# Kernel tuning notes

Measured on AMD Instinct MI355X. Metric: run time of the kernel, lower is better.

The kernel has to match this reference:

```python
import jax, jax.numpy as jnp
import numpy as np

B, T, STEPS = 4096, 56, 28
H, ANN, ENC, DEC = 126, 30, 20, 15
DIN = 1 + DEC + H  # decoder GRU input width = 142


def _gru_step(h, x, Wih, Whh, bih, bhh):
    # torch GRU cell math; Wih: [3H, in], Whh: [3H, H]
    gi = x @ Wih.T + bih
    gh = h @ Whh.T + bhh
    ir, iz, inn = jnp.split(gi, 3, axis=-1)
    hr, hz, hn = jnp.split(gh, 3, axis=-1)
    r = jax.nn.sigmoid(ir + hr)
    z = jax.nn.sigmoid(iz + hz)
    n = jnp.tanh(inn + r * hn)
    return (1.0 - z) * n + z * h


def setup_inputs() -> dict:
    key = jax.random.key(0)
    ks = jax.random.split(key, 23)
    p = lambda k, s: jax.random.normal(k, s, dtype=jnp.float32) * 0.08
    return {
        "ann_data": jax.random.normal(ks[0], (B, ANN), dtype=jnp.float32),
        "encoder_data": jax.random.normal(ks[1], (T, B, ENC), dtype=jnp.float32),
        "decoder_data": jax.random.normal(ks[2], (STEPS, B, DEC), dtype=jnp.float32),
        "s2h_W1": p(ks[3], (96, ANN)), "s2h_b1": p(ks[4], (96,)),
        "s2h_W2": p(ks[5], (H, 96)), "s2h_b2": p(ks[6], (H,)),
        "enc_Wih": p(ks[7], (3 * H, ENC)), "enc_Whh": p(ks[8], (3 * H, H)),
        "enc_bih": p(ks[9], (3 * H,)), "enc_bhh": p(ks[10], (3 * H,)),
        "dec_Wih": p(ks[11], (3 * H, DIN)), "dec_Whh": p(ks[12], (3 * H, H)),
        "dec_bih": p(ks[13], (3 * H,)), "dec_bhh": p(ks[14], (3 * H,)),
        "U_W": p(ks[15], (H, H)), "U_b": p(ks[16], (H,)),
        "Wl_W": p(ks[17], (H, H)), "Wl_b": p(ks[18], (H,)),
        "V_W": p(ks[19], (1, H)), "V_b": p(ks[20], (1,)),
        "h2o_W": p(ks[21], (1, H)), "h2o_b": p(ks[22], (1,)),
    }


def reference(ann_data, encoder_data, decoder_data,
              s2h_W1, s2h_b1, s2h_W2, s2h_b2,
              enc_Wih, enc_Whh, enc_bih, enc_bhh,
              dec_Wih, dec_Whh, dec_bih, dec_bhh,
              U_W, U_b, Wl_W, Wl_b, V_W, V_b, h2o_W, h2o_b):
    # static -> initial hidden: Linear(ANN,96) -> ReLU -> Linear(96,H)
    hidden = jnp.maximum(ann_data @ s2h_W1.T + s2h_b1, 0.0) @ s2h_W2.T + s2h_b2  # [B,H]

    def enc_f(h, x):
        h2 = _gru_step(h, x, enc_Wih, enc_Whh, enc_bih, enc_bhh)
        return h2, h2

    hidden, enc_out = jax.lax.scan(enc_f, hidden, encoder_data)  # enc_out: [T,B,H]

    Uo = enc_out @ U_W.T + U_b            # [T,B,H] precomputed (loop-invariant)
    gt0 = encoder_data[-1, :, 0:1]        # initial_ground, [B,1]

    def dec_f(carry, dec_x):
        h, prev = carry
        Wh = h @ Wl_W.T + Wl_b                              # [B,H]
        scores = jnp.tanh(Uo + Wh[None]) @ V_W.T + V_b      # [T,B,1]
        alpha = jax.nn.softmax(scores, axis=0)              # softmax over time
        attn = jnp.einsum('tb,tbh->bh', alpha[..., 0], enc_out)
        x = jnp.concatenate([prev, dec_x, attn], axis=1)    # [B,DIN]
        h2 = _gru_step(h, x, dec_Wih, dec_Whh, dec_bih, dec_bhh)
        out = h2 @ h2o_W.T + h2o_b                          # [B,1]
        return (h2, out), out

    _, outputs = jax.lax.scan(dec_f, (hidden, gt0), decoder_data)
    return outputs  # [STEPS, B, 1]
```

## Files before the change

### kernel.cpp

```cpp
#include <hip/hip_runtime.h>
#include <stdint.h>

typedef unsigned int u32;
typedef unsigned short u16;
typedef _Float16 f16;
typedef _Float16 f16x8 __attribute__((ext_vector_type(8)));
typedef _Float16 f16x4 __attribute__((ext_vector_type(4)));
typedef _Float16 f16x2 __attribute__((ext_vector_type(2)));
typedef float f32x4 __attribute__((ext_vector_type(4)));

constexpr int NB = 4096;
constexpr int NT = 56;
constexpr int NS = 28;
constexpr int NH = 126;
constexpr int NHP = 128;
constexpr float LOG2E = 1.4426950408889634f;

constexpr int LROW = 136;
constexpr int LB   = NT * LROW + 8;

constexpr int TJP = 120;
constexpr int TB  = 7712;

constexpr size_t OFF_H    = 0;
constexpr size_t OFF_ENC  = 2097152;
constexpr size_t OFF_UO   = OFF_ENC + 58720256;
constexpr size_t OFF_WENC = OFF_UO + 58720256;
constexpr size_t OFF_WDEC = OFF_WENC + 122880;
constexpr size_t OFF_WL   = OFF_WDEC + 221184;
constexpr size_t OFF_UW   = OFF_WL + 32768;

__device__ __forceinline__ float fexp2(float x){ return __builtin_amdgcn_exp2f(x); }
__device__ __forceinline__ float frcp (float x){ return __builtin_amdgcn_rcpf(x); }
__device__ __forceinline__ float sigm (float x){ return frcp(1.f + fexp2(-LOG2E * x)); }
__device__ __forceinline__ float ftanh(float x){ return 1.f - 2.f * frcp(1.f + fexp2(2.f * LOG2E * x)); }
__device__ __forceinline__ float asf(u32 u){ union { u32 i; float f; } v; v.i = u; return v.f; }
__device__ __forceinline__ u16 tobf(float f){ union { float f; u32 i; } v; v.f = f;
  return (u16)((v.i + 0x7fffu + ((v.i >> 16) & 1u)) >> 16); }

__global__ void k_prep(const float* __restrict__ eWih, const float* __restrict__ eWhh,
                       const float* __restrict__ dWih, const float* __restrict__ dWhh,
                       const float* __restrict__ UW,   const float* __restrict__ Wl,
                       char* __restrict__ ws)
{
  f16* wenc = (f16*)(ws + OFF_WENC);
  f16* wdec = (f16*)(ws + OFF_WDEC);
  f16* wl   = (f16*)(ws + OFF_WL);
  f16* uw   = (f16*)(ws + OFF_UW);
  const int nE = 384 * 160, nD = 384 * 288, nW = 128 * 128;
  const int total = nE + nD + nW + nW;
  for (int i = blockIdx.x * 256 + threadIdx.x; i < total; i += gridDim.x * 256) {
    int idx = i;
    if (idx < nE) {
      const int r = idx / 160, c = idx % 160;
      float v = 0.f;
      if (r < 378) {
        if (c < 20) v = eWih[r * 20 + c];
        else if (c >= 32 && c < 158) v = eWhh[r * 126 + (c - 32)];
      }
      wenc[idx] = (f16)v; continue;
    }
    idx -= nE;
    if (idx < nD) {
      const int r = idx / 288, c = idx % 288;
      float v = 0.f;
      if (r < 378) {
        if (c < 16) v = dWih[r * 142 + c];
        else if (c >= 32 && c < 158) v = dWih[r * 142 + 16 + (c - 32)];
        else if (c >= 160 && c < 286) v = dWhh[r * 126 + (c - 160)];
      }
      wdec[idx] = (f16)v; continue;
    }
    idx -= nD;
    if (idx < nW) {
      const int r = idx >> 7, c = idx & 127;
      wl[idx] = (f16)((r < 126 && c < 126) ? Wl[r * 126 + c] : 0.f);
      continue;
    }
    idx -= nW;
    { const int r = idx >> 7, c = idx & 127;
      uw[idx] = (f16)((r < 126 && c < 126) ? UW[r * 126 + c] : 0.f); }
  }
}

__global__ __launch_bounds__(256) void k_mlp(
    const float* __restrict__ ann, const float* __restrict__ W1, const float* __restrict__ b1,
    const float* __restrict__ W2, const float* __restrict__ b2, float* __restrict__ hstate)
{
  __shared__ float anns[32][33];
  __shared__ float t1s[32][101];
  const int tid = threadIdx.x;
  const int b0 = blockIdx.x * 32;
  for (int i = tid; i < 32 * 30; i += 256)
    anns[i / 30][i % 30] = ann[(b0 + i / 30) * 30 + (i % 30)];
  __syncthreads();
  const int b = tid & 31, rg = tid >> 5;
  for (int m = rg; m < 96; m += 8) {
    float a = b1[m];
    for (int k = 0; k < 30; ++k) a += W1[m * 30 + k] * anns[b][k];
    t1s[b][m] = fmaxf(a, 0.f);
  }
  __syncthreads();
  for (int j = rg; j < NHP; j += 8) {
    float a = 0.f;
    if (j < NH) {
      a = b2[j];
      for (int k = 0; k < 96; ++k) a += W2[j * 96 + k] * t1s[b][k];
    }
    hstate[(b0 + b) * NHP + j] = a;
  }
}

__global__ __launch_bounds__(512) void k_enc(
    const float* __restrict__ xenc, const f16* __restrict__ Wenc,
    const f16* __restrict__ Uw,
    const float* __restrict__ bih, const float* __restrict__ bhh,
    const float* __restrict__ Ub,
    float* __restrict__ hstate, f16* __restrict__ encO, u16* __restrict__ uoO)
{
  __shared__ f16 av[16][296];
  const int tid = threadIdx.x;
  const int wid = tid >> 6, l = tid & 63, quad = l >> 4, col = l & 15;
  const int b0 = blockIdx.x * 16;
  const int jb = wid * 16, j = jb + col;
  const bool valid = j < NH;
  const int jc = valid ? j : NH - 1;

  const float br  = bih[jc]        + bhh[jc];
  const float bz  = bih[NH + jc]   + bhh[NH + jc];
  const float bnx = bih[2*NH + jc];
  const float bnh = bhh[2*NH + jc];
  const float ub  = Ub[jc];

  f16x8 rB[5], zB[5], nxB, nhB[4], uB[4];
  {
    const int ko = quad * 8, rr = jb + col;
#pragma unroll
    for (int kt = 0; kt < 5; ++kt) {
      rB[kt] = *(const f16x8*)&Wenc[rr * 160 + kt * 32 + ko];
      zB[kt] = *(const f16x8*)&Wenc[(NH + rr) * 160 + kt * 32 + ko];
    }
    nxB = *(const f16x8*)&Wenc[(2*NH + rr) * 160 + ko];
#pragma unroll
    for (int kt = 0; kt < 4; ++kt) {
      nhB[kt] = *(const f16x8*)&Wenc[(2*NH + rr) * 160 + 32 + kt * 32 + ko];
      uB[kt]  = *(const f16x8*)&Uw[rr * 128 + kt * 32 + ko];
    }
  }

  {
    const int bb = tid >> 5, c4 = (tid & 31) * 4;
    const float4 hv = *(const float4*)&hstate[(b0 + bb) * NHP + c4];
    av[bb][32 + c4]     = (f16)hv.x; av[bb][32 + c4 + 1] = (f16)hv.y;
    av[bb][32 + c4 + 2] = (f16)hv.z; av[bb][32 + c4 + 3] = (f16)hv.w;
  }
  if (tid < 192) { const int bb = tid / 12, p = tid % 12; av[bb][20 + p] = (f16)0.f; }
  __syncthreads();

  const int m = col, ko = quad * 8;
  for (int t = 0; t < NT; ++t) {
    const int hp = 32 + (t & 1) * 128, hq = 32 + ((t + 1) & 1) * 128;
    if (tid < 320) {
      const int bb = tid / 20, e = tid % 20;
      av[bb][e] = (f16)xenc[((size_t)t * NB + b0 + bb) * 20 + e];
    }
    __syncthreads();
    f16x8 A[5];
    A[0] = *(const f16x8*)&av[m][ko];
#pragma unroll
    for (int kt = 1; kt < 5; ++kt) A[kt] = *(const f16x8*)&av[m][hp + (kt - 1) * 32 + ko];

    f32x4 Cr = {br, br, br, br}, Cz = {bz, bz, bz, bz};
    f32x4 Cnx = {bnx, bnx, bnx, bnx}, Cnh = {bnh, bnh, bnh, bnh};
#pragma unroll
    for (int kt = 0; kt < 5; ++kt) {
      Cr = __builtin_amdgcn_mfma_f32_16x16x32_f16(A[kt], rB[kt], Cr, 0, 0, 0);
      Cz = __builtin_amdgcn_mfma_f32_16x16x32_f16(A[kt], zB[kt], Cz, 0, 0, 0);
    }
    Cnx = __builtin_amdgcn_mfma_f32_16x16x32_f16(A[0], nxB, Cnx, 0, 0, 0);
#pragma unroll
    for (int kt = 0; kt < 4; ++kt)
      Cnh = __builtin_amdgcn_mfma_f32_16x16x32_f16(A[kt + 1], nhB[kt], Cnh, 0, 0, 0);

    float hv4[4];
#pragma unroll
    for (int c = 0; c < 4; ++c) {
      const int bb = quad * 4 + c;
      const float hold = (float)av[bb][hp + j];
      const float r = sigm(Cr[c]), z = sigm(Cz[c]);
      const float n = ftanh(Cnx[c] + r * Cnh[c]);
      hv4[c] = (1.f - z) * n + z * hold;
    }
#pragma unroll
    for (int c = 0; c < 4; ++c) {
      const int bb = quad * 4 + c;
      const f16 hs = valid ? (f16)hv4[c] : (f16)0.f;
      av[bb][hq + j] = hs;
      encO[((size_t)(b0 + bb) * NT + t) * 128 + j] = hs;
    }
    if (t == NT - 1 && valid) {
#pragma unroll
      for (int c = 0; c < 4; ++c)
        hstate[(b0 + quad * 4 + c) * NHP + j] = hv4[c];
    }
    __syncthreads();

    f16x8 Ah[4];
#pragma unroll
    for (int kt = 0; kt < 4; ++kt) Ah[kt] = *(const f16x8*)&av[m][hq + kt * 32 + ko];
    f32x4 Cu = {ub, ub, ub, ub};
#pragma unroll
    for (int kt = 0; kt < 4; ++kt)
      Cu = __builtin_amdgcn_mfma_f32_16x16x32_f16(Ah[kt], uB[kt], Cu, 0, 0, 0);
#pragma unroll
    for (int c = 0; c < 4; ++c) {
      const u16 eu = tobf(fexp2(2.f * LOG2E * Cu[c]));
      uoO[((size_t)(b0 + quad * 4 + c) * NT + t) * 128 + j] = valid ? eu : (u16)0;
    }
  }
}

__global__ __launch_bounds__(512) void k_dec(
    const float* __restrict__ xdec, const float* __restrict__ xenc,
    const f16* __restrict__ Wdec, const f16* __restrict__ WlW,
    const float* __restrict__ bih, const float* __restrict__ bhh,
    const float* __restrict__ Wlb, const float* __restrict__ Vw,
    const float* __restrict__ Vb, const float* __restrict__ how,
    const float* __restrict__ hob, const float* __restrict__ hstate,
    const f16* __restrict__ encO, const u16* __restrict__ uoO,
    float* __restrict__ out)
{
  __shared__ __align__(16) u16 uoL[4 * LB];
  __shared__ __align__(16) f16 encT[4 * TB];
  __shared__ __align__(16) f16 av[5][424];
  __shared__ float EWS[4][132];
  __shared__ float scS[4][60];
  __shared__ __align__(16) f16 hows16[128];
  const int tid = threadIdx.x;
  const int wid = tid >> 6, l = tid & 63, quad = l >> 4, col = l & 15;
  const int b0 = blockIdx.x * 4;
  const int jb = wid * 16, j = jb + col;
  const bool valid = j < NH;
  const int jc = valid ? j : NH - 1;

  const float br  = bih[jc]        + bhh[jc];
  const float bz  = bih[NH + jc]   + bhh[NH + jc];
  const float bnx = bih[2*NH + jc];
  const float bnh = bhh[2*NH + jc];
  const float wb  = Wlb[jc];
  const float vb0 = Vb[0], hob0 = hob[0];

  f16x8 rB[9], zB[9], nxB[5], nhB[4], wlB[4];
  {
    const int ko = quad * 8, rr = jb + col;
#pragma unroll
    for (int kt = 0; kt < 9; ++kt) {
      rB[kt] = *(const f16x8*)&Wdec[rr * 288 + kt * 32 + ko];
      zB[kt] = *(const f16x8*)&Wdec[(NH + rr) * 288 + kt * 32 + ko];
    }
#pragma unroll
    for (int kt = 0; kt < 5; ++kt)
      nxB[kt] = *(const f16x8*)&Wdec[(2*NH + rr) * 288 + kt * 32 + ko];
#pragma unroll
    for (int kt = 0; kt < 4; ++kt) {
      nhB[kt] = *(const f16x8*)&Wdec[(2*NH + rr) * 288 + 160 + kt * 32 + ko];
      wlB[kt] = *(const f16x8*)&WlW[rr * 128 + kt * 32 + ko];
    }
  }

  const int g = tid >> 3, sub = tid & 7;
  float n2v[16], svsum = 0.f;
#pragma unroll
  for (int i = 0; i < 16; ++i) {
    const int jj = sub * 16 + i;
    const float v = (jj < NH) ? Vw[jj] : 0.f;
    n2v[i] = -2.f * v;
    svsum += v;
  }
  if (tid >= 256 && tid < 384) {
    const int q = tid - 256; hows16[q] = (f16)((q < NH) ? how[q] : 0.f);
  }
  for (int i = tid; i < 5 * 424; i += 512) av[i / 424][i % 424] = (f16)0.f;
  if (tid < 24) EWS[tid / 6][126 + tid % 6] = 0.f;
  {
    const size_t gb = (size_t)b0 * NT * 128;
    for (int i = tid; i < 4 * NT * 16; i += 512) {
      const int ch = i & 15, btr = i >> 4;
      const int bb = btr / NT, tt = btr % NT;
      const size_t src = gb + (size_t)btr * 128 + ch * 8;
      *(f16x8*)&uoL[bb * LB + tt * LROW + ch * 8] = *(const f16x8*)&uoO[src];
      const f16x8 ev = *(const f16x8*)&encO[src];
#pragma unroll
      for (int k2 = 0; k2 < 4; ++k2) {
        f16x2 pr; pr[0] = ev[2 * k2]; pr[1] = ev[2 * k2 + 1];
        *(f16x2*)&encT[bb * TB + (ch * 4 + k2) * TJP + tt * 2] = pr;
      }
    }
  }
  __syncthreads();
  if (tid < 128) {
    const int bb = tid >> 5, c4 = (tid & 31) * 4;
    const float4 hv = *(const float4*)&hstate[(b0 + bb) * NHP + c4];
    av[bb][160 + c4]     = (f16)hv.x; av[bb][160 + c4 + 1] = (f16)hv.y;
    av[bb][160 + c4 + 2] = (f16)hv.z; av[bb][160 + c4 + 3] = (f16)hv.w;
  }
  if (tid < 4) av[tid][0] = (f16)xenc[((size_t)(NT - 1) * NB + b0 + tid) * 20];
  __syncthreads();

  const int m = col, ko = quad * 8;
  const int arow = ((m & 3) == 0) ? (m >> 2) : 4;
  const int pb = tid & 3, pth = (tid >> 2) & 1, pjp = tid >> 3;

  for (int s = 0; s < NS; ++s) {
    const int hp = 160 + (s & 1) * 128, hq = 160 + ((s + 1) & 1) * 128;

    {
      f16x8 Ah[4];
#pragma unroll
      for (int kt = 0; kt < 4; ++kt) Ah[kt] = *(const f16x8*)&av[arow][hp + kt * 32 + ko];
      f32x4 Cw = {wb, wb, wb, wb};
#pragma unroll
      for (int kt = 0; kt < 4; ++kt)
        Cw = __builtin_amdgcn_mfma_f32_16x16x32_f16(Ah[kt], wlB[kt], Cw, 0, 0, 0);
      if (valid) EWS[quad][j] = fexp2(2.f * LOG2E * Cw[0]);
    }
    if (tid < 60) { const int bb = tid / 15, e = tid % 15;
      av[bb][1 + e] = (f16)xdec[((size_t)s * NB + b0 + bb) * 15 + e]; }
    __syncthreads();

    {
      const int sbb = g & 3, tb = g >> 2;
      float ew[16];
#pragma unroll
      for (int i = 0; i < 4; ++i)
        *(float4*)&ew[i * 4] = *(const float4*)&EWS[sbb][sub * 16 + i * 4];
      const u16* up0 = &uoL[sbb * LB + sub * 16];
      uint4 q0 = *(const uint4*)&up0[tb * LROW];
      uint4 q1 = *(const uint4*)&up0[tb * LROW + 8];
#pragma unroll
      for (int rd = 0; rd < 4; ++rd) {
        const int t = rd * 16 + tb;
        const u32 wsv[8] = {q0.x, q0.y, q0.z, q0.w, q1.x, q1.y, q1.z, q1.w};
        if (rd < 3) {
          const int tn = (t + 16 < NT) ? (t + 16) : (NT - 1);
          q0 = *(const uint4*)&up0[tn * LROW];
          q1 = *(const uint4*)&up0[tn * LROW + 8];
        }
        if (t < NT) {
          float ac0 = 0.f, ac1 = 0.f, ac2 = 0.f, ac3 = 0.f;
#pragma unroll
          for (int k = 0; k < 8; k += 2) {
            const float p0 = fmaf(asf(wsv[k]     << 16),          ew[2 * k],     1.f);
            const float p1 = fmaf(asf(wsv[k]     & 0xffff0000u),  ew[2 * k + 1], 1.f);
            const float p2 = fmaf(asf(wsv[k + 1] << 16),          ew[2 * k + 2], 1.f);
            const float p3 = fmaf(asf(wsv[k + 1] & 0xffff0000u),  ew[2 * k + 3], 1.f);
            ac0 = fmaf(n2v[2 * k],     frcp(p0), ac0);
            ac1 = fmaf(n2v[2 * k + 1], frcp(p1), ac1);
            ac2 = fmaf(n2v[2 * k + 2], frcp(p2), ac2);
            ac3 = fmaf(n2v[2 * k + 3], frcp(p3), ac3);
          }
          float acc = svsum + (ac0 + ac1) + (ac2 + ac3);
          acc += __shfl_xor(acc, 1, 64);
          acc += __shfl_xor(acc, 2, 64);
          acc += __shfl_xor(acc, 4, 64);
          if (sub == 0) scS[sbb][t] = fexp2(LOG2E * (acc + vb0));
        }
      }
    }
    __syncthreads();

    {
      const int j0 = pjp * 2;
      const f16* er = &encT[pb * TB + pjp * TJP + pth * 56];
      const float* scp = &scS[pb][pth * 28];
      float Za = 0.f, Zb = 0.f;
      float a0a = 0.f, a0b = 0.f, a1a = 0.f, a1b = 0.f;
#pragma unroll
      for (int it = 0; it < 7; ++it) {
        const f16x8 ev = *(const f16x8*)&er[it * 8];
        const float4 sc = *(const float4*)&scp[it * 4];
        Za += sc.x; Zb += sc.y; Za += sc.z; Zb += sc.w;
        a0a = fmaf(sc.x, (float)ev[0], a0a);
        a1a = fmaf(sc.x, (float)ev[1], a1a);
        a0b = fmaf(sc.y, (float)ev[2], a0b);
        a1b = fmaf(sc.y, (float)ev[3], a1b);
        a0a = fmaf(sc.z, (float)ev[4], a0a);
        a1a = fmaf(sc.z, (float)ev[5], a1a);
        a0b = fmaf(sc.w, (float)ev[6], a0b);
        a1b = fmaf(sc.w, (float)ev[7], a1b);
      }
      float Z = Za + Zb, a0 = a0a + a0b, a1 = a1a + a1b;
      a0 += __shfl_xor(a0, 4, 64);
      a1 += __shfl_xor(a1, 4, 64);
      Z  += __shfl_xor(Z, 4, 64);
      if (pth == 0) {
        const float inv = frcp(Z);
        f16x2 st; st[0] = (f16)(a0 * inv); st[1] = (f16)(a1 * inv);
        *(f16x2*)&av[pb][32 + j0] = st;
      }
    }
    __syncthreads();

    {
      f16x8 A[9];
#pragma unroll
      for (int kt = 0; kt < 5; ++kt) A[kt] = *(const f16x8*)&av[arow][kt * 32 + ko];
#pragma unroll
      for (int kt = 5; kt < 9; ++kt) A[kt] = *(const f16x8*)&av[arow][hp + (kt - 5) * 32 + ko];
      f32x4 Cr = {br, br, br, br}, Cz = {bz, bz, bz, bz};
      f32x4 Cnx = {bnx, bnx, bnx, bnx}, Cnh = {bnh, bnh, bnh, bnh};
#pragma unroll
      for (int kt = 0; kt < 9; ++kt) {
        Cr = __builtin_amdgcn_mfma_f32_16x16x32_f16(A[kt], rB[kt], Cr, 0, 0, 0);
        Cz = __builtin_amdgcn_mfma_f32_16x16x32_f16(A[kt], zB[kt], Cz, 0, 0, 0);
      }
#pragma unroll
      for (int kt = 0; kt < 5; ++kt)
        Cnx = __builtin_amdgcn_mfma_f32_16x16x32_f16(A[kt], nxB[kt], Cnx, 0, 0, 0);
#pragma unroll
      for (int kt = 0; kt < 4; ++kt)
        Cnh = __builtin_amdgcn_mfma_f32_16x16x32_f16(A[kt + 5], nhB[kt], Cnh, 0, 0, 0);
      {
        const float hold = (float)av[quad][hp + j];
        const float r = sigm(Cr[0]), z = sigm(Cz[0]);
        const float n = ftanh(Cnx[0] + r * Cnh[0]);
        const float h2 = (1.f - z) * n + z * hold;
        if (valid) av[quad][hq + j] = (f16)h2;
      }
    }
    __syncthreads();

    if (wid == 0) {
      f16x8 Ah2[4], hB[4];
      const f16x8 zz = {};
#pragma unroll
      for (int kt = 0; kt < 4; ++kt) {
        Ah2[kt] = *(const f16x8*)&av[arow][hq + kt * 32 + ko];
        hB[kt] = (col == 0) ? *(const f16x8*)&hows16[kt * 32 + ko] : zz;
      }
      f32x4 Co = {0.f, 0.f, 0.f, 0.f};
#pragma unroll
      for (int kt = 0; kt < 4; ++kt)
        Co = __builtin_amdgcn_mfma_f32_16x16x32_f16(Ah2[kt], hB[kt], Co, 0, 0, 0);
      if (col == 0) {
        const float o = Co[0] + hob0;
        out[(size_t)s * NB + b0 + quad] = o;
        av[quad][0] = (f16)o;
      }
    }
  }
}

extern "C" void kernel_launch(void* const* d_in, const int* in_sizes, int n_in,
                              void* d_out, int out_size, void* d_ws, size_t ws_size,
                              hipStream_t stream)
{
  const float* ann   = (const float*)d_in[0];
  const float* xenc  = (const float*)d_in[1];
  const float* xdec  = (const float*)d_in[2];
  const float* W1    = (const float*)d_in[3];
  const float* b1    = (const float*)d_in[4];
  const float* W2    = (const float*)d_in[5];
  const float* b2    = (const float*)d_in[6];
  const float* eWih  = (const float*)d_in[7];
  const float* eWhh  = (const float*)d_in[8];
  const float* ebih  = (const float*)d_in[9];
  const float* ebhh  = (const float*)d_in[10];
  const float* dWih  = (const float*)d_in[11];
  const float* dWhh  = (const float*)d_in[12];
  const float* dbih  = (const float*)d_in[13];
  const float* dbhh  = (const float*)d_in[14];
  const float* UW    = (const float*)d_in[15];
  const float* Ubias = (const float*)d_in[16];
  const float* Wl    = (const float*)d_in[17];
  const float* Wlb   = (const float*)d_in[18];
  const float* Vw    = (const float*)d_in[19];
  const float* Vb    = (const float*)d_in[20];
  const float* how   = (const float*)d_in[21];
  const float* hob   = (const float*)d_in[22];

  char* ws = (char*)d_ws;
  float* hstate = (float*)(ws + OFF_H);
  f16*   encB   = (f16*)(ws + OFF_ENC);
  u16*   uoB    = (u16*)(ws + OFF_UO);
  const f16* pWenc = (const f16*)(ws + OFF_WENC);
  const f16* pWdec = (const f16*)(ws + OFF_WDEC);
  const f16* pWl   = (const f16*)(ws + OFF_WL);
  const f16* pUW   = (const f16*)(ws + OFF_UW);

  k_prep<<<200, 256, 0, stream>>>(eWih, eWhh, dWih, dWhh, UW, Wl, ws);
  k_mlp <<<128, 256, 0, stream>>>(ann, W1, b1, W2, b2, hstate);
  k_enc <<<NB / 16, 512, 0, stream>>>(xenc, pWenc, pUW, ebih, ebhh, Ubias,
                                      hstate, encB, uoB);
  k_dec <<<NB / 4, 512, 0, stream>>>(xdec, xenc, pWdec, pWl, dbih, dbhh,
                                     Wlb, Vw, Vb, how, hob, hstate,
                                     encB, uoB, (float*)d_out);
}
```

Before: 596.6 us.

## Fuse output projection into next step's attention phase and batch score reductions

Drops the separate barrier-delimited output projection phase at the end of each decoder step. Wave 0 now computes the previous step's h2o output while it does the Wl projection, reusing the same loaded hidden-state A fragments, and the last step's output is handled after the loop. The score loop now batches the cross-lane shuffle reductions across all four time rounds instead of reducing each round in turn. The Uo exponent cache moves from bf16 to f16 storage, unpacked with native f16 converts, and k_dec gets a minimum-occupancy hint of two blocks per CU. The f16 cache lowers range headroom for exp values, and the occupancy hint may force register spills.

```diff
diff --git a/kernel.cpp b/kernel.cpp
--- a/kernel.cpp
+++ b/kernel.cpp
@@ -34,9 +34,6 @@
 __device__ __forceinline__ float frcp (float x){ return __builtin_amdgcn_rcpf(x); }
 __device__ __forceinline__ float sigm (float x){ return frcp(1.f + fexp2(-LOG2E * x)); }
 __device__ __forceinline__ float ftanh(float x){ return 1.f - 2.f * frcp(1.f + fexp2(2.f * LOG2E * x)); }
-__device__ __forceinline__ float asf(u32 u){ union { u32 i; float f; } v; v.i = u; return v.f; }
-__device__ __forceinline__ u16 tobf(float f){ union { float f; u32 i; } v; v.f = f;
-  return (u16)((v.i + 0x7fffu + ((v.i >> 16) & 1u)) >> 16); }
 
 __global__ void k_prep(const float* __restrict__ eWih, const float* __restrict__ eWhh,
                        const float* __restrict__ dWih, const float* __restrict__ dWhh,
@@ -214,13 +211,14 @@
       Cu = __builtin_amdgcn_mfma_f32_16x16x32_f16(Ah[kt], uB[kt], Cu, 0, 0, 0);
 #pragma unroll
     for (int c = 0; c < 4; ++c) {
-      const u16 eu = tobf(fexp2(2.f * LOG2E * Cu[c]));
-      uoO[((size_t)(b0 + quad * 4 + c) * NT + t) * 128 + j] = valid ? eu : (u16)0;
+      union { f16 h; u16 u; } cv;
+      cv.h = (f16)fexp2(2.f * LOG2E * Cu[c]);
+      uoO[((size_t)(b0 + quad * 4 + c) * NT + t) * 128 + j] = valid ? cv.u : (u16)0;
     }
   }
 }
 
-__global__ __launch_bounds__(512) void k_dec(
+__global__ __launch_bounds__(512, 2) void k_dec(
     const float* __restrict__ xdec, const float* __restrict__ xenc,
     const f16* __restrict__ Wdec, const f16* __restrict__ WlW,
     const float* __restrict__ bih, const float* __restrict__ bhh,
@@ -323,6 +321,22 @@
       for (int kt = 0; kt < 4; ++kt)
         Cw = __builtin_amdgcn_mfma_f32_16x16x32_f16(Ah[kt], wlB[kt], Cw, 0, 0, 0);
       if (valid) EWS[quad][j] = fexp2(2.f * LOG2E * Cw[0]);
+      if (wid == 0 && s > 0) {
+        f16x8 hB[4];
+        const f16x8 zz = {};
+#pragma unroll
+        for (int kt = 0; kt < 4; ++kt)
+          hB[kt] = (col == 0) ? *(const f16x8*)&hows16[kt * 32 + ko] : zz;
+        f32x4 Co = {0.f, 0.f, 0.f, 0.f};
+#pragma unroll
+        for (int kt = 0; kt < 4; ++kt)
+          Co = __builtin_amdgcn_mfma_f32_16x16x32_f16(Ah[kt], hB[kt], Co, 0, 0, 0);
+        if (col == 0) {
+          const float o = Co[0] + hob0;
+          out[(size_t)(s - 1) * NB + b0 + quad] = o;
+          av[quad][0] = (f16)o;
+        }
+      }
     }
     if (tid < 60) { const int bb = tid / 15, e = tid % 15;
       av[bb][1 + e] = (f16)xdec[((size_t)s * NB + b0 + bb) * 15 + e]; }
@@ -337,6 +351,7 @@
       const u16* up0 = &uoL[sbb * LB + sub * 16];
       uint4 q0 = *(const uint4*)&up0[tb * LROW];
       uint4 q1 = *(const uint4*)&up0[tb * LROW + 8];
+      float rs[4];
 #pragma unroll
       for (int rd = 0; rd < 4; ++rd) {
         const int t = rd * 16 + tb;
@@ -346,24 +361,39 @@
           q0 = *(const uint4*)&up0[tn * LROW];
           q1 = *(const uint4*)&up0[tn * LROW + 8];
         }
-        if (t < NT) {
-          float ac0 = 0.f, ac1 = 0.f, ac2 = 0.f, ac3 = 0.f;
-#pragma unroll
-          for (int k = 0; k < 8; k += 2) {
-            const float p0 = fmaf(asf(wsv[k]     << 16),          ew[2 * k],     1.f);
-            const float p1 = fmaf(asf(wsv[k]     & 0xffff0000u),  ew[2 * k + 1], 1.f);
-            const float p2 = fmaf(asf(wsv[k + 1] << 16),          ew[2 * k + 2], 1.f);
-            const float p3 = fmaf(asf(wsv[k + 1] & 0xffff0000u),  ew[2 * k + 3], 1.f);
-            ac0 = fmaf(n2v[2 * k],     frcp(p0), ac0);
-            ac1 = fmaf(n2v[2 * k + 1], frcp(p1), ac1);
-            ac2 = fmaf(n2v[2 * k + 2], frcp(p2), ac2);
-            ac3 = fmaf(n2v[2 * k + 3], frcp(p3), ac3);
-          }
-          float acc = svsum + (ac0 + ac1) + (ac2 + ac3);
-          acc += __shfl_xor(acc, 1, 64);
-          acc += __shfl_xor(acc, 2, 64);
-          acc += __shfl_xor(acc, 4, 64);
-          if (sub == 0) scS[sbb][t] = fexp2(LOG2E * (acc + vb0));
+        float ac0 = 0.f, ac1 = 0.f, ac2 = 0.f, ac3 = 0.f;
+#pragma unroll
+        for (int k = 0; k < 8; k += 2) {
+          union { u32 i; f16x2 h; } ua, ub2;
+          ua.i = wsv[k]; ub2.i = wsv[k + 1];
+          const float p0 = fmaf((float)ua.h[0],  ew[2 * k],     1.f);
+          const float p1 = fmaf((float)ua.h[1],  ew[2 * k + 1], 1.f);
+          const float p2 = fmaf((float)ub2.h[0], ew[2 * k + 2], 1.f);
+          const float p3 = fmaf((float)ub2.h[1], ew[2 * k + 3], 1.f);
+          ac0 = fmaf(n2v[2 * k],     frcp(p0), ac0);
+          ac1 = fmaf(n2v[2 * k + 1], frcp(p1), ac1);
+          ac2 = fmaf(n2v[2 * k + 2], frcp(p2), ac2);
+          ac3 = fmaf(n2v[2 * k + 3], frcp(p3), ac3);
+        }
+        rs[rd] = svsum + (ac0 + ac1) + (ac2 + ac3);
+      }
+      rs[0] += __shfl_xor(rs[0], 1, 64);
+      rs[1] += __shfl_xor(rs[1], 1, 64);
+      rs[2] += __shfl_xor(rs[2], 1, 64);
+      rs[3] += __shfl_xor(rs[3], 1, 64);
+      rs[0] += __shfl_xor(rs[0], 2, 64);
+      rs[1] += __shfl_xor(rs[1], 2, 64);
+      rs[2] += __shfl_xor(rs[2], 2, 64);
+      rs[3] += __shfl_xor(rs[3], 2, 64);
+      rs[0] += __shfl_xor(rs[0], 4, 64);
+      rs[1] += __shfl_xor(rs[1], 4, 64);
+      rs[2] += __shfl_xor(rs[2], 4, 64);
+      rs[3] += __shfl_xor(rs[3], 4, 64);
+      if (sub == 0) {
+#pragma unroll
+        for (int rd = 0; rd < 4; ++rd) {
+          const int t = rd * 16 + tb;
+          if (t < NT) scS[sbb][t] = fexp2(LOG2E * (rs[rd] + vb0));
         }
       }
     }
@@ -429,25 +459,22 @@
       }
     }
     __syncthreads();
-
-    if (wid == 0) {
-      f16x8 Ah2[4], hB[4];
-      const f16x8 zz = {};
-#pragma unroll
-      for (int kt = 0; kt < 4; ++kt) {
-        Ah2[kt] = *(const f16x8*)&av[arow][hq + kt * 32 + ko];
-        hB[kt] = (col == 0) ? *(const f16x8*)&hows16[kt * 32 + ko] : zz;
-      }
-      f32x4 Co = {0.f, 0.f, 0.f, 0.f};
-#pragma unroll
-      for (int kt = 0; kt < 4; ++kt)
-        Co = __builtin_amdgcn_mfma_f32_16x16x32_f16(Ah2[kt], hB[kt], Co, 0, 0, 0);
-      if (col == 0) {
-        const float o = Co[0] + hob0;
-        out[(size_t)s * NB + b0 + quad] = o;
-        av[quad][0] = (f16)o;
-      }
-    }
+  }
+
+  if (wid == 0) {
+    const int hql = 160 + (NS & 1) * 128;
+    f16x8 Ah2[4], hB[4];
+    const f16x8 zz = {};
+#pragma unroll
+    for (int kt = 0; kt < 4; ++kt) {
+      Ah2[kt] = *(const f16x8*)&av[arow][hql + kt * 32 + ko];
+      hB[kt] = (col == 0) ? *(const f16x8*)&hows16[kt * 32 + ko] : zz;
+    }
+    f32x4 Co = {0.f, 0.f, 0.f, 0.f};
+#pragma unroll
+    for (int kt = 0; kt < 4; ++kt)
+      Co = __builtin_amdgcn_mfma_f32_16x16x32_f16(Ah2[kt], hB[kt], Co, 0, 0, 0);
+    if (col == 0) out[(size_t)(NS - 1) * NB + b0 + quad] = Co[0] + hob0;
   }
 }
 
```

Result: faster. 584.7 us (-2.0%).
